# Optimization experiments

Measured on AMD Instinct MI355X. Metric: run time of the kernel, lower is better.

The kernel has to match this reference:

```python
import jax, jax.numpy as jnp
import numpy as np

B = 32768
T = 30
H = 384


def setup_inputs() -> dict:
    key = jax.random.key(0)
    ks = jax.random.split(key, 16)

    def lin(k, out_d, in_d):
        # torch nn.Linear init: U(-1/sqrt(in_d), 1/sqrt(in_d))
        bound = 1.0 / np.sqrt(in_d)
        kw, kb = jax.random.split(k)
        W = jax.random.uniform(kw, (out_d, in_d), jnp.float32, -bound, bound)
        b = jax.random.uniform(kb, (out_d,), jnp.float32, -bound, bound)
        return W, b

    Wp, bp = lin(ks[0], 128, 3)        # plan_input
    Ws, bs = lin(ks[1], 128, 3)        # state_input
    # GRUCell params: weight_ih [3H,128], weight_hh [3H,H], init U(-1/sqrt(H),..)
    gb = 1.0 / np.sqrt(H)
    W_ih = jax.random.uniform(ks[2], (3 * H, 128), jnp.float32, -gb, gb)
    b_ih = jax.random.uniform(ks[3], (3 * H,), jnp.float32, -gb, gb)
    W_hh = jax.random.uniform(ks[4], (3 * H, H), jnp.float32, -gb, gb)
    b_hh = jax.random.uniform(ks[5], (3 * H,), jnp.float32, -gb, gb)
    Wd1, bd1 = lin(ks[6], 64, H)       # decode Linear(384,64)
    Wd2, bd2 = lin(ks[7], 3, 64)       # decode Linear(64,3)

    init_hidden = jax.random.normal(ks[8], (B, H), jnp.float32)
    plan = jax.random.normal(ks[9], (B, T, 3), jnp.float32)
    gate = jax.random.uniform(ks[10], (B, 1), jnp.float32)
    init_state = jax.random.normal(ks[11], (B, 3), jnp.float32)

    return {
        "init_hidden": init_hidden, "plan": plan, "gate": gate,
        "init_state": init_state,
        "Wp": Wp, "bp": bp, "Ws": Ws, "bs": bs,
        "W_ih": W_ih, "b_ih": b_ih, "W_hh": W_hh, "b_hh": b_hh,
        "Wd1": Wd1, "bd1": bd1, "Wd2": Wd2, "bd2": bd2,
    }


def reference(init_hidden, plan, gate, init_state,
              Wp, bp, Ws, bs, W_ih, b_ih, W_hh, b_hh,
              Wd1, bd1, Wd2, bd2):
    # Dropout(0.1) is identity in eval mode.
    plan_seq = jnp.swapaxes(plan[:, :T, :3], 0, 1)  # [T,B,3]

    def step(carry, plan_t):
        hidden, state = carry  # [B,H], [B,3]
        x = (state @ Ws.T + bs) + (plan_t @ Wp.T + bp) * gate  # [B,128]
        gi = x @ W_ih.T + b_ih          # [B,3H]
        gh = hidden @ W_hh.T + b_hh     # [B,3H]
        ir, iz, inn = jnp.split(gi, 3, axis=-1)
        hr, hz, hn = jnp.split(gh, 3, axis=-1)
        r = jax.nn.sigmoid(ir + hr)
        z = jax.nn.sigmoid(iz + hz)
        n = jnp.tanh(inn + r * hn)
        hidden = (1.0 - z) * n + z * hidden
        dec = jax.nn.elu(hidden @ Wd1.T + bd1) @ Wd2.T + bd2  # [B,3]
        state = dec + state
        return (hidden, state), state

    _, outs = jax.lax.scan(step, (init_hidden, init_state[:, :3]), plan_seq)
    return jnp.swapaxes(outs, 0, 1)  # [B,T,3]
```

## Files before the change

### kernel.cpp

```cpp
#include <hip/hip_runtime.h>


#define TT  30
#define NPH 50
#define PHU 12288
#define HPU 6144
#define STRU 614400
#define HS  392

typedef unsigned short u16;
typedef __bf16 bf16x8 __attribute__((ext_vector_type(8)));
typedef u16    u16x8  __attribute__((ext_vector_type(8)));
typedef float  f32x16 __attribute__((ext_vector_type(16)));

__device__ __forceinline__ u16 f2b(float f){
  unsigned u = __float_as_uint(f);
  u += 0x7FFFu + ((u >> 16) & 1u);
  return (u16)(u >> 16);
}
__device__ __forceinline__ float b2f(u16 h){ return __uint_as_float(((unsigned)h) << 16); }

__device__ __forceinline__ f32x16 mfma32(u16x8 a, u16x8 b, f32x16 c){
  return __builtin_amdgcn_mfma_f32_32x32x16_bf16(
      __builtin_bit_cast(bf16x8, a), __builtin_bit_cast(bf16x8, b), c, 0, 0, 0);
}
__device__ __forceinline__ void lds_fence(){
  asm volatile("s_waitcnt lgkmcnt(0)" ::: "memory");
  __builtin_amdgcn_sched_barrier(0);
}
__device__ __forceinline__ float sigf(float x){ return __builtin_amdgcn_rcpf(1.f + __expf(-x)); }
__device__ __forceinline__ float tanh_(float x){ return 2.f*__builtin_amdgcn_rcpf(1.f + __expf(-2.f*x)) - 1.f; }

__device__ __forceinline__ void stage16(const u16* g, u16* l){
  __builtin_amdgcn_global_load_lds(
      (const __attribute__((address_space(1))) unsigned int*)g,
      (__attribute__((address_space(3))) unsigned int*)l, 16, 0, 0);
}

__global__ void prep_kernel(const float* __restrict__ Wih, const float* __restrict__ Whh,
                            const float* __restrict__ Wd1, const float* __restrict__ Wd2,
                            const float* __restrict__ bih, const float* __restrict__ bhh,
                            const float* __restrict__ Ws,  const float* __restrict__ bs,
                            const float* __restrict__ Wp,  const float* __restrict__ bp,
                            u16* __restrict__ stream, u16* __restrict__ wd2p,
                            u16* __restrict__ wxp, float* __restrict__ gb)
{
  int i = blockIdx.x*blockDim.x + threadIdx.x;
  if (i < 442368){
    int row = i/384, k = i - row*384;
    int g = row/384, unit = row - g*384, c = unit>>5, lc = unit&31;
    int kf = k>>4, hl = (k>>3)&1, j = k&7;
    int phase = c*4 + 1 + g;
    stream[(size_t)phase*PHU + kf*512 + (lc+32*hl)*8 + j] = f2b(Whh[i]);
  }
  if (i < 147456){
    int row = i>>7, k = i&127;
    int g = row/384, unit = row - g*384, c = unit>>5, lc = unit&31;
    int kf = k>>4, hl = (k>>3)&1, j = k&7;
    int phase = c*4;
    stream[(size_t)phase*PHU + (g*8+kf)*512 + (lc+32*hl)*8 + j] = f2b(Wih[i]);
  }
  if (i < 24576){
    int row = i/384, k = i - row*384;
    int ct = row>>5, lc = row&31;
    int kf = k>>4, hl = (k>>3)&1, j = k&7;
    int phase = 48 + ct;
    stream[(size_t)phase*PHU + kf*512 + (lc+32*hl)*8 + j] = f2b(Wd1[i]);
  }
  if (i < 2048){
    int kf = i>>9, r = i&511;
    int n = (r>>3)&31, hl = r>>8, j = r&7;
    int k = kf*16 + hl*8 + j;
    wd2p[i] = f2b((n<3) ? Wd2[n*64 + k] : 0.f);
  }
  if (i < 2048){
    int tl = i>>9, r = i&511;
    int n = (r>>3)&31, hl = r>>8, j = r&7;
    int k = hl*8 + j, u = tl*32 + n;
    float v = 0.f;
    if      (k <= 2) v = Ws[u*3 + k];
    else if (k == 3) v = bs[u];
    else if (k <= 6) v = Wp[u*3 + (k-4)];
    else if (k == 7) v = bp[u];
    wxp[i] = f2b(v);
  }
  if (i < 384){
    gb[i*4+0] = bih[i]       + bhh[i];
    gb[i*4+1] = bih[384+i]   + bhh[384+i];
    gb[i*4+2] = bih[768+i];
    gb[i*4+3] = bhh[768+i];
  }
}

__global__ __launch_bounds__(256, 1)
void gru_main(const float* __restrict__ ih, const float* __restrict__ plan,
              const float* __restrict__ gate, const float* __restrict__ istate,
              const u16* __restrict__ stream, const u16* __restrict__ wd2p,
              const u16* __restrict__ wxp, const float* __restrict__ gb,
              const float* __restrict__ bd1, const float* __restrict__ bd2,
              float* __restrict__ out)
{
  __shared__ __attribute__((aligned(16))) u16 wb[5*HPU];
  __shared__ __attribute__((aligned(16))) u16 hn[4][32*HS];

  const int tid  = threadIdx.x;
  const int wave = tid >> 6, lane = tid & 63;
  const int m    = lane & 31, hl = lane >> 5;
  const int R0   = blockIdx.x*128 + wave*32;
  u16* hw = hn[wave];

  const float gt    = gate[R0 + m];
  const float bd1v0 = bd1[m], bd1v1 = bd1[32+m];
  const float bd2v  = (m<3) ? bd2[m] : 0.f;

  if (lane < 32){
    const float* sp = istate + (size_t)(R0+lane)*3;
    float* q = (float*)&hw[lane*HS + 384];
    q[0]=sp[0]; q[1]=sp[1]; q[2]=sp[2]; q[3]=0.f;
  }

  u16x8 hold[24];
#pragma unroll
  for (int kf=0; kf<24; ++kf){
    const float* p = ih + (size_t)(R0+m)*384 + kf*16 + hl*8;
    float4 a = *(const float4*)p;
    float4 b = *(const float4*)(p+4);
    u16x8 v;
    v[0]=f2b(a.x); v[1]=f2b(a.y); v[2]=f2b(a.z); v[3]=f2b(a.w);
    v[4]=f2b(b.x); v[5]=f2b(b.y); v[6]=f2b(b.z); v[7]=f2b(b.w);
    hold[kf]=v;
    *(u16x8*)&hw[m*HS + kf*16 + hl*8] = v;
  }

  int hoff = 0;
  int ss   = 0;
  int sa   = 0, sb = 1;
  auto stage_half = [&](){
    const u16* s = stream + hoff + wave*1536 + lane*8;
    u16* d = &wb[ss*HPU + wave*1536];
    stage16(s,        d);
    stage16(s + 512,  d + 512);
    stage16(s + 1024, d + 1024);
    hoff += HPU; if (hoff == STRU) hoff = 0;
    ss = (ss==4) ? 0 : ss+1;
  };
  auto phase_end = [&](){
    asm volatile("s_waitcnt vmcnt(3) lgkmcnt(0)" ::: "memory");
    __builtin_amdgcn_sched_barrier(0);
    __builtin_amdgcn_s_barrier();
    __builtin_amdgcn_sched_barrier(0);
    sa = (sa>=3) ? sa-3 : sa+2;
    sb = (sb>=3) ? sb-3 : sb+2;
  };
  auto preload = [&](u16x8* bf){
    const u16* W0 = wb + sa*HPU + lane*8;
    const u16* W1 = wb + sb*HPU + lane*8;
#pragma unroll
    for (int f=0; f<12; ++f) bf[f]      = *(const u16x8*)(W0 + f*512);
#pragma unroll
    for (int f=0; f<12; ++f) bf[12+f]   = *(const u16x8*)(W1 + f*512);
  };

  stage_half(); stage_half(); stage_half();
  asm volatile("s_waitcnt vmcnt(3) lgkmcnt(0)" ::: "memory");
  __builtin_amdgcn_sched_barrier(0);
  __builtin_amdgcn_s_barrier();
  __builtin_amdgcn_sched_barrier(0);

#pragma unroll 1
  for (int t=0; t<TT; ++t){
    u16x8 a8;
    {
      float4 sv = *(const float4*)&hw[m*HS + 384];
      const float* pp = plan + (size_t)(R0+m)*(TT*3) + t*3;
      float f0=sv.x, f1=sv.y, f2=sv.z, f3=1.f;
      float f4=gt*pp[0], f5=gt*pp[1], f6=gt*pp[2], f7=gt;
      if (hl){ a8[0]=0;a8[1]=0;a8[2]=0;a8[3]=0;a8[4]=0;a8[5]=0;a8[6]=0;a8[7]=0; }
      else { a8[0]=f2b(f0);a8[1]=f2b(f1);a8[2]=f2b(f2);a8[3]=f2b(f3);
             a8[4]=f2b(f4);a8[5]=f2b(f5);a8[6]=f2b(f6);a8[7]=f2b(f7); }
    }
    u16x8 xf[8];
#pragma unroll
    for (int tl=0; tl<4; ++tl){
      f32x16 ax;
#pragma unroll
      for (int r=0;r<16;++r) ax[r]=0.f;
      ax = mfma32(a8, *(const u16x8*)(wxp + tl*512 + lane*8), ax);
#pragma unroll
      for (int r=0;r<16;++r){
        int row = (r&3) + ((r>>2)<<3) + 4*hl;
        hw[row*HS + m] = f2b(ax[r]);
      }
      lds_fence();
      xf[2*tl]   = *(const u16x8*)&hw[m*HS + hl*8];
      xf[2*tl+1] = *(const u16x8*)&hw[m*HS + 16 + hl*8];
      lds_fence();
    }
    *(u16x8*)&hw[m*HS + hl*8]      = hold[0];
    *(u16x8*)&hw[m*HS + 16 + hl*8] = hold[1];
    lds_fence();

#pragma unroll 1
    for (int c=0; c<12; ++c){
      f32x16 aR, aZ, aNI, aNH;
      {
        const float4 b4 = *(const float4*)(gb + (size_t)(c*32+m)*4);
#pragma unroll
        for (int r=0;r<16;++r){ aR[r]=b4.x; aZ[r]=b4.y; aNI[r]=b4.z; aNH[r]=b4.w; }
      }
      {
        stage_half(); stage_half();
        u16x8 bf[24]; preload(bf);
#pragma unroll
        for (int kf=0; kf<8; ++kf){
          aR  = mfma32(xf[kf], bf[kf],    aR);
          aZ  = mfma32(xf[kf], bf[8+kf],  aZ);
          aNI = mfma32(xf[kf], bf[16+kf], aNI);
        }
        phase_end();
      }
      {
        stage_half(); stage_half();
        u16x8 bf[24]; preload(bf);
#pragma unroll
        for (int kf=0; kf<24; ++kf)
          aR = mfma32(hold[kf], bf[kf], aR);
        phase_end();
      }
      {
        stage_half(); stage_half();
        u16x8 bf[24]; preload(bf);
#pragma unroll
        for (int kf=0; kf<24; ++kf)
          aZ = mfma32(hold[kf], bf[kf], aZ);
        phase_end();
      }
      {
        stage_half(); stage_half();
        u16x8 bf[24]; preload(bf);
#pragma unroll
        for (int kf=0; kf<24; ++kf)
          aNH = mfma32(hold[kf], bf[kf], aNH);
#pragma unroll
        for (int r=0;r<16;++r){
          int row = (r&3) + ((r>>2)<<3) + 4*hl;
          float rr = sigf(aR[r]);
          float zz = sigf(aZ[r]);
          float nn = tanh_(aNI[r] + rr*aNH[r]);
          int off = row*HS + c*32 + m;
          float ho = b2f(hw[off]);
          hw[off] = f2b((1.f-zz)*nn + zz*ho);
        }
        phase_end();
      }
    }

    lds_fence();
#pragma unroll
    for (int kf=0; kf<24; ++kf)
      hold[kf] = *(const u16x8*)&hw[m*HS + kf*16 + hl*8];

    f32x16 a0, a1;
#pragma unroll
    for (int r=0;r<16;++r){ a0[r]=bd1v0; a1[r]=bd1v1; }
    {
      stage_half(); stage_half();
      u16x8 bf[24]; preload(bf);
#pragma unroll
      for (int kf=0; kf<24; ++kf)
        a0 = mfma32(hold[kf], bf[kf], a0);
      phase_end();
    }
    {
      stage_half(); stage_half();
      u16x8 bf[24]; preload(bf);
#pragma unroll
      for (int kf=0; kf<24; ++kf)
        a1 = mfma32(hold[kf], bf[kf], a1);

      u16x8 wd2f0 = *(const u16x8*)(wd2p + 0*512 + lane*8);
      u16x8 wd2f1 = *(const u16x8*)(wd2p + 1*512 + lane*8);
      u16x8 wd2f2 = *(const u16x8*)(wd2p + 2*512 + lane*8);
      u16x8 wd2f3 = *(const u16x8*)(wd2p + 3*512 + lane*8);

      f32x16 ao;
#pragma unroll
      for (int r=0;r<16;++r) ao[r]=0.f;
#pragma unroll
      for (int r=0;r<16;++r){
        int row = (r&3) + ((r>>2)<<3) + 4*hl;
        float e = a0[r]; e = e>0.f ? e : (__expf(e)-1.f);
        hw[row*HS + m] = f2b(e);
      }
      lds_fence();
      {
        u16x8 af0 = *(const u16x8*)&hw[m*HS + hl*8];
        u16x8 af1 = *(const u16x8*)&hw[m*HS + 16 + hl*8];
        ao = mfma32(af0, wd2f0, ao);
        ao = mfma32(af1, wd2f1, ao);
      }
      lds_fence();
#pragma unroll
      for (int r=0;r<16;++r){
        int row = (r&3) + ((r>>2)<<3) + 4*hl;
        float e = a1[r]; e = e>0.f ? e : (__expf(e)-1.f);
        hw[row*HS + m] = f2b(e);
      }
      lds_fence();
      {
        u16x8 af0 = *(const u16x8*)&hw[m*HS + hl*8];
        u16x8 af1 = *(const u16x8*)&hw[m*HS + 16 + hl*8];
        ao = mfma32(af0, wd2f2, ao);
        ao = mfma32(af1, wd2f3, ao);
      }
      lds_fence();
      *(u16x8*)&hw[m*HS + hl*8]      = hold[0];
      *(u16x8*)&hw[m*HS + 16 + hl*8] = hold[1];

#pragma unroll
      for (int r=0;r<16;++r){
        int row = (r&3) + ((r>>2)<<3) + 4*hl;
        if (m < 3){
          float* q = (float*)&hw[row*HS + 384];
          float ns = q[m] + ao[r] + bd2v;
          out[(size_t)(R0+row)*(TT*3) + t*3 + m] = ns;
          q[m] = ns;
        }
      }
      phase_end();
    }
  }
}

extern "C" void kernel_launch(void* const* d_in, const int* in_sizes, int n_in,
                              void* d_out, int out_size, void* d_ws, size_t ws_size,
                              hipStream_t stream)
{
  (void)in_sizes; (void)n_in; (void)out_size; (void)ws_size;
  const float* ih     = (const float*)d_in[0];
  const float* plan   = (const float*)d_in[1];
  const float* gatep  = (const float*)d_in[2];
  const float* istate = (const float*)d_in[3];
  const float* Wp     = (const float*)d_in[4];
  const float* bp     = (const float*)d_in[5];
  const float* Ws     = (const float*)d_in[6];
  const float* bs     = (const float*)d_in[7];
  const float* Wih    = (const float*)d_in[8];
  const float* bih    = (const float*)d_in[9];
  const float* Whh    = (const float*)d_in[10];
  const float* bhh    = (const float*)d_in[11];
  const float* Wd1    = (const float*)d_in[12];
  const float* bd1    = (const float*)d_in[13];
  const float* Wd2    = (const float*)d_in[14];
  const float* bd2    = (const float*)d_in[15];

  u16*   wstream = (u16*)d_ws;
  u16*   wd2p    = (u16*)((char*)d_ws + 1228800);
  u16*   wxp     = (u16*)((char*)d_ws + 1232896);
  float* gb      = (float*)((char*)d_ws + 1236992);

  prep_kernel<<<1728, 256, 0, stream>>>(Wih, Whh, Wd1, Wd2, bih, bhh, Ws, bs, Wp, bp,
                                        wstream, wd2p, wxp, gb);
  gru_main<<<256, 256, 0, stream>>>(ih, plan, gatep, istate,
                                    wstream, wd2p, wxp, gb, bd1, bd2, (float*)d_out);
}
```

Before: 1.598 ms.

## Double-buffer LDS weight fragments in registers to overlap preload with MFMA

Instead of loading each phase's weight fragments from LDS right before using them, the kernel now keeps two register buffers. The next phase's fragments are preloaded while the current phase's MFMAs run on the other buffer. This is meant to hide LDS read latency behind matrix math. It doubles the register footprint for weight fragments (48 u16x8) and adds a prologue that stages and preloads the first phase, with ring indices shifted accordingly.

```diff
diff --git a/kernel.cpp b/kernel.cpp
--- a/kernel.cpp
+++ b/kernel.cpp
@@ -92,6 +92,27 @@
   }
 }
 
+#define PRELOAD(BN) { \
+  const u16* W0_ = wb + ra*HPU + lane*8; \
+  const u16* W1_ = wb + rb*HPU + lane*8; \
+  _Pragma("unroll") for (int f_=0; f_<12; ++f_) BN[f_]    = *(const u16x8*)(W0_ + f_*512); \
+  _Pragma("unroll") for (int f_=0; f_<12; ++f_) BN[12+f_] = *(const u16x8*)(W1_ + f_*512); }
+
+#define PH_GH(ACC, BC, BN) { \
+  stage_half(); stage_half(); \
+  PRELOAD(BN); \
+  _Pragma("unroll") for (int kf_=0; kf_<24; ++kf_) ACC = mfma32(hold[kf_], BC[kf_], ACC); \
+  phase_end(); }
+
+#define PH_GI(BC, BN) { \
+  stage_half(); stage_half(); \
+  PRELOAD(BN); \
+  _Pragma("unroll") for (int kf_=0; kf_<8; ++kf_){ \
+    aR  = mfma32(xf[kf_], BC[kf_],    aR); \
+    aZ  = mfma32(xf[kf_], BC[8+kf_],  aZ); \
+    aNI = mfma32(xf[kf_], BC[16+kf_], aNI); } \
+  phase_end(); }
+
 __global__ __launch_bounds__(256, 1)
 void gru_main(const float* __restrict__ ih, const float* __restrict__ plan,
               const float* __restrict__ gate, const float* __restrict__ istate,
@@ -134,7 +155,7 @@
 
   int hoff = 0;
   int ss   = 0;
-  int sa   = 0, sb = 1;
+  int ra   = 0, rb = 1;
   auto stage_half = [&](){
     const u16* s = stream + hoff + wave*1536 + lane*8;
     u16* d = &wb[ss*HPU + wave*1536];
@@ -149,23 +170,24 @@
     __builtin_amdgcn_sched_barrier(0);
     __builtin_amdgcn_s_barrier();
     __builtin_amdgcn_sched_barrier(0);
-    sa = (sa>=3) ? sa-3 : sa+2;
-    sb = (sb>=3) ? sb-3 : sb+2;
+    ra = (ra>=3) ? ra-3 : ra+2;
+    rb = (rb>=3) ? rb-3 : rb+2;
   };
-  auto preload = [&](u16x8* bf){
-    const u16* W0 = wb + sa*HPU + lane*8;
-    const u16* W1 = wb + sb*HPU + lane*8;
-#pragma unroll
-    for (int f=0; f<12; ++f) bf[f]      = *(const u16x8*)(W0 + f*512);
-#pragma unroll
-    for (int f=0; f<12; ++f) bf[12+f]   = *(const u16x8*)(W1 + f*512);
-  };
-
+
+  u16x8 bfA[24], bfB[24];
+
+  stage_half(); stage_half();
+  asm volatile("s_waitcnt vmcnt(0)" ::: "memory");
+  __builtin_amdgcn_sched_barrier(0);
+  __builtin_amdgcn_s_barrier();
+  __builtin_amdgcn_sched_barrier(0);
+  PRELOAD(bfA);
   stage_half(); stage_half(); stage_half();
   asm volatile("s_waitcnt vmcnt(3) lgkmcnt(0)" ::: "memory");
   __builtin_amdgcn_sched_barrier(0);
   __builtin_amdgcn_s_barrier();
   __builtin_amdgcn_sched_barrier(0);
+  ra = 2; rb = 3;
 
 #pragma unroll 1
   for (int t=0; t<TT; ++t){
@@ -208,39 +230,15 @@
 #pragma unroll
         for (int r=0;r<16;++r){ aR[r]=b4.x; aZ[r]=b4.y; aNI[r]=b4.z; aNH[r]=b4.w; }
       }
+      PH_GI(bfA, bfB);
+      PH_GH(aR, bfB, bfA);
+      PH_GH(aZ, bfA, bfB);
       {
         stage_half(); stage_half();
-        u16x8 bf[24]; preload(bf);
-#pragma unroll
-        for (int kf=0; kf<8; ++kf){
-          aR  = mfma32(xf[kf], bf[kf],    aR);
-          aZ  = mfma32(xf[kf], bf[8+kf],  aZ);
-          aNI = mfma32(xf[kf], bf[16+kf], aNI);
-        }
-        phase_end();
-      }
-      {
-        stage_half(); stage_half();
-        u16x8 bf[24]; preload(bf);
+        PRELOAD(bfA);
 #pragma unroll
         for (int kf=0; kf<24; ++kf)
-          aR = mfma32(hold[kf], bf[kf], aR);
-        phase_end();
-      }
-      {
-        stage_half(); stage_half();
-        u16x8 bf[24]; preload(bf);
-#pragma unroll
-        for (int kf=0; kf<24; ++kf)
-          aZ = mfma32(hold[kf], bf[kf], aZ);
-        phase_end();
-      }
-      {
-        stage_half(); stage_half();
-        u16x8 bf[24]; preload(bf);
-#pragma unroll
-        for (int kf=0; kf<24; ++kf)
-          aNH = mfma32(hold[kf], bf[kf], aNH);
+          aNH = mfma32(hold[kf], bfB[kf], aNH);
 #pragma unroll
         for (int r=0;r<16;++r){
           int row = (r&3) + ((r>>2)<<3) + 4*hl;
@@ -263,20 +261,13 @@
     f32x16 a0, a1;
 #pragma unroll
     for (int r=0;r<16;++r){ a0[r]=bd1v0; a1[r]=bd1v1; }
+    PH_GH(a0, bfA, bfB);
     {
       stage_half(); stage_half();
-      u16x8 bf[24]; preload(bf);
+      PRELOAD(bfA);
 #pragma unroll
       for (int kf=0; kf<24; ++kf)
-        a0 = mfma32(hold[kf], bf[kf], a0);
-      phase_end();
-    }
-    {
-      stage_half(); stage_half();
-      u16x8 bf[24]; preload(bf);
-#pragma unroll
-      for (int kf=0; kf<24; ++kf)
-        a1 = mfma32(hold[kf], bf[kf], a1);
+        a1 = mfma32(hold[kf], bfB[kf], a1);
 
       u16x8 wd2f0 = *(const u16x8*)(wd2p + 0*512 + lane*8);
       u16x8 wd2f1 = *(const u16x8*)(wd2p + 1*512 + lane*8);
```

New measurement: 1.645 ms. 2.9% more time.
